# Performance work log

Measured on AMD Instinct MI355X. Metric: run time of the kernel, lower is better.

Reference implementation:

```python
import jax, jax.numpy as jnp
import numpy as np

B, H, W, C = 2, 192, 192, 192
WS, SHIFT, NH = 16, 8, 6


def _window_partition(x, ws):
    b, h, w, c = x.shape
    x = x.reshape(b, h // ws, ws, w // ws, ws, c)
    return x.transpose(0, 1, 3, 2, 4, 5).reshape(-1, ws, ws, c)


def _window_reverse(win, ws, h, w):
    b = win.shape[0] // ((h // ws) * (w // ws))
    x = win.reshape(b, h // ws, w // ws, ws, ws, -1)
    return x.transpose(0, 1, 3, 2, 4, 5).reshape(b, h, w, -1)


def _relative_position_index(ws):
    coords = np.stack(np.meshgrid(np.arange(ws), np.arange(ws), indexing="ij"))
    cf = coords.reshape(2, -1)
    rel = (cf[:, :, None] - cf[:, None, :]).transpose(1, 2, 0).astype(np.int64)
    rel[..., 0] += ws - 1
    rel[..., 1] += ws - 1
    rel[..., 0] *= 2 * ws - 1
    return rel.sum(-1)  # (ws*ws, ws*ws) in [0, (2ws-1)^2)


def _shift_attn_mask(h, w, ws, shift):
    img = np.zeros((1, h, w, 1), np.float32)
    cnt = 0
    for hs in (slice(0, -ws), slice(-ws, -shift), slice(-shift, None)):
        for wsl in (slice(0, -ws), slice(-ws, -shift), slice(-shift, None)):
            img[:, hs, wsl, :] = cnt
            cnt += 1
    mw = np.asarray(_window_partition(jnp.asarray(img), ws)).reshape(-1, ws * ws)
    diff = mw[:, None, :] - mw[:, :, None]
    return jnp.asarray(np.where(diff != 0, -100.0, 0.0).astype(np.float32))


def setup_inputs():
    key = jax.random.key(0)
    ks = jax.random.split(key, 4)
    x = jax.random.normal(ks[0], (B, H, W, C), jnp.float32)
    qkv = jax.random.normal(ks[1], (B, H, W, 3 * C), jnp.float32)
    rpb_table = 0.02 * jax.random.normal(ks[2], ((2 * WS - 1) ** 2, NH), jnp.float32)
    geo_scale = jnp.full((NH,), 0.01, jnp.float32)
    geo_sigma = jnp.asarray(1.0, jnp.float32)
    proj_w = 0.02 * jax.random.normal(ks[3], (C, C), jnp.float32)
    proj_b = jnp.zeros((C,), jnp.float32)
    rpi = jnp.asarray(_relative_position_index(WS), jnp.int32)
    attn_mask = _shift_attn_mask(H, W, WS, SHIFT)
    return dict(x=x, qkv=qkv, rpb_table=rpb_table, geo_scale=geo_scale,
                geo_sigma=geo_sigma, proj_w=proj_w, proj_b=proj_b,
                rpi=rpi, attn_mask=attn_mask,
                window_size=WS, shift_size=SHIFT, num_heads=NH)


def _geo_bias(f, ws, sigma):
    # f: (nwb, ws, ws, C). L-shaped geodesic path: horizontal then vertical cumsums.
    nwb = f.shape[0]
    diff_h = jnp.sum(jnp.abs(f[:, :, 1:] - f[:, :, :-1]), -1)  # (nwb, ws, ws-1)
    ct_h = jnp.cumsum(jnp.concatenate(
        [jnp.zeros((nwb, ws, 1), f.dtype), 1.0 + sigma * diff_h], -1), -1)
    diff_v = jnp.sum(jnp.abs(f[:, 1:] - f[:, :-1]), -1)        # (nwb, ws-1, ws)
    ct_v = jnp.cumsum(jnp.concatenate(
        [jnp.zeros((nwb, 1, ws), f.dtype), 1.0 + sigma * diff_v], -2), -2)
    idx = jnp.arange(ws * ws)
    rows, cols = idx // ws, idx % ws
    ct_h_flat = ct_h[:, rows, cols]                    # (nwb, n)
    ct_v_flat = ct_v[:, rows, cols]
    ct_h_corner = ct_h[:, rows[:, None], cols[None, :]]  # ct_h[ri, cj] -> (nwb, n, n)
    ct_v_corner = ct_v[:, rows[:, None], cols[None, :]]
    geo_h = jnp.abs(ct_h_corner - ct_h_flat[:, :, None])
    geo_v = jnp.abs(ct_v_flat[:, None, :] - ct_v_corner)
    return geo_h + geo_v                               # (nwb, n, n)


def _forward(x, qkv, rpb_table, geo_scale, geo_sigma, proj_w, proj_b,
             rpi, attn_mask, ws, shift, nh):
    b, h, w, c = x.shape
    n = ws * ws
    hd = c // nh
    sx = jnp.roll(x, (-shift, -shift), (1, 2))
    sqkv = jnp.roll(qkv, (-shift, -shift), (1, 2))
    f_win = _window_partition(sx, ws)                           # (nwb, ws, ws, c)
    geo = _geo_bias(f_win, ws, jnp.abs(geo_sigma))              # (nwb, n, n)
    qkv_win = _window_partition(sqkv, ws).reshape(-1, n, 3, nh, hd)
    q = qkv_win[:, :, 0].transpose(0, 2, 1, 3)                  # (nwb, nh, n, hd)
    k = qkv_win[:, :, 1].transpose(0, 2, 1, 3)
    v = qkv_win[:, :, 2].transpose(0, 2, 1, 3)
    attn = jnp.einsum("bhqd,bhkd->bhqk", q * (hd ** -0.5), k)   # (nwb, nh, n, n)
    rpb = rpb_table[rpi.reshape(-1)].reshape(n, n, nh).transpose(2, 0, 1)
    attn = attn + rpb[None]
    attn = attn - geo[:, None] * geo_scale[None, :, None, None]
    nw = attn_mask.shape[0]
    attn = attn.reshape(b, nw, nh, n, n) + attn_mask[None, :, None]
    attn = jax.nn.softmax(attn.reshape(-1, nh, n, n), axis=-1)
    out = jnp.einsum("bhqk,bhkd->bqhd", attn, v).reshape(-1, n, c)
    out = out @ proj_w.T + proj_b                               # nn.Linear
    out = _window_reverse(out.reshape(-1, ws, ws, c), ws, h, w)
    out = jnp.roll(out, (shift, shift), (1, 2))
    return out.reshape(b, h * w, c)


def reference(x, qkv, rpb_table, geo_scale, geo_sigma, proj_w, proj_b,
              rpi, attn_mask, window_size, shift_size, num_heads):
    return _forward(x, qkv, rpb_table, geo_scale, geo_sigma, proj_w, proj_b,
                    rpi, attn_mask, window_size, shift_size, num_heads)
```

## Files before the change

kernel.cpp:

```cpp
#include <hip/hip_runtime.h>
#include <stdint.h>

#define HH 192
#define WWW 192
#define CC 192
#define WS 16
#define SHIFTS 8
#define NH 6
#define HD 32
#define NN 256
#define NWS 12
#define NWIN_B 144
#define NWIN 288
#define CTN (NWIN * NN)

typedef _Float16 half_t;
typedef half_t half2_t __attribute__((ext_vector_type(2)));
typedef half_t f16x8 __attribute__((ext_vector_type(8)));
typedef float f32x4 __attribute__((ext_vector_type(4)));

#define LOG2E 1.4426950408889634f

#if __has_builtin(__builtin_amdgcn_exp2f)
#define EXP2F(x) __builtin_amdgcn_exp2f(x)
#else
#define EXP2F(x) __expf(0.6931471805599453f * (x))
#endif

__device__ __forceinline__ float sat16(float a) {
    return fminf(fmaxf(a, -60000.f), 60000.f);
}
__device__ __forceinline__ uint32_t pack_h2(float a, float b) {
    half2_t h; h.x = (half_t)sat16(a); h.y = (half_t)sat16(b);
    return __builtin_bit_cast(uint32_t, h);
}

__device__ __forceinline__ size_t xrow(int b, int sh, int sw) {
    int oh = sh + SHIFTS; if (oh >= HH) oh -= HH;
    int ow = sw + SHIFTS; if (ow >= WWW) ow -= WWW;
    return ((size_t)((b * HH + oh) * WWW + ow)) * CC;
}
__device__ __forceinline__ size_t qkvrow(int b, int sh, int sw) {
    int oh = sh + SHIFTS; if (oh >= HH) oh -= HH;
    int ow = sw + SHIFTS; if (ow >= WWW) ow -= WWW;
    return ((size_t)((b * HH + oh) * WWW + ow)) * (3 * CC);
}
__device__ __forceinline__ int regof(int v) { return v < (HH - WS) ? 0 : (v < (HH - SHIFTS) ? 1 : 2); }

__device__ __forceinline__ float* ctptr(float* o, int q) {
    int slot = q / 96;
    int off = q - slot * 96;
    return o + (size_t)slot * CC + 96 + off;
}

__global__ __launch_bounds__(256) void kgeo(const float* __restrict__ x,
                                            const float* __restrict__ sigp,
                                            float* __restrict__ outbuf) {
    __shared__ float dh[16][16];
    __shared__ float dv[16][16];
    int win = blockIdx.x;
    int b = win / NWIN_B, wi = win % NWIN_B;
    int wr = wi / NWS, wc = wi % NWS;
    int t = threadIdx.x;
    int r = t >> 4, j = t & 15;
    int r1 = (r < 15) ? r + 1 : r;
    int j1 = (j < 15) ? j + 1 : j;

    const float4* a4 = (const float4*)(x + xrow(b, wr * WS + r,  wc * WS + j));
    const float4* b4 = (const float4*)(x + xrow(b, wr * WS + r,  wc * WS + j1));
    const float4* c4 = (const float4*)(x + xrow(b, wr * WS + r1, wc * WS + j));
    float sh_ = 0.f, sv_ = 0.f;
    #pragma unroll 4
    for (int ch = 0; ch < 48; ch++) {
        float4 fa = a4[ch], fb = b4[ch], fc = c4[ch];
        sh_ += fabsf(fb.x - fa.x) + fabsf(fb.y - fa.y) + fabsf(fb.z - fa.z) + fabsf(fb.w - fa.w);
        sv_ += fabsf(fc.x - fa.x) + fabsf(fc.y - fa.y) + fabsf(fc.z - fa.z) + fabsf(fc.w - fa.w);
    }
    dh[r][j] = (j < 15) ? sh_ : 0.f;
    dv[r][j] = (r < 15) ? sv_ : 0.f;
    __syncthreads();

    float sigma = fabsf(sigp[0]);
    if (t < 16) {
        float acc = 0.f;
        *ctptr(outbuf, win * NN + t * 16) = 0.f;
        for (int jj = 1; jj < 16; jj++) {
            acc += 1.0f + sigma * dh[t][jj - 1];
            *ctptr(outbuf, win * NN + t * 16 + jj) = acc;
        }
    } else if (t < 32) {
        int c = t - 16;
        float acc = 0.f;
        *ctptr(outbuf, CTN + win * NN + c) = 0.f;
        for (int ii = 1; ii < 16; ii++) {
            acc += 1.0f + sigma * dv[ii - 1][c];
            *ctptr(outbuf, CTN + win * NN + ii * 16 + c) = acc;
        }
    }
}

__global__ __launch_bounds__(512, 4) void kattn(const float* __restrict__ qkv,
                                                const float* __restrict__ rpb_table,
                                                const float* __restrict__ geo_scale,
                                                float* __restrict__ outbuf) {
    __shared__ __align__(16) uint32_t Klds[256 * 20];
    __shared__ __align__(16) uint32_t Vt[32 * 140];
    __shared__ __align__(16) uint32_t Pbuf[8 * 32 * 20];
    __shared__ float cth_s[NN], ctv_s[NN];
    __shared__ float rpb_s[961];

    int win = blockIdx.x, head = blockIdx.y;
    int b = win / NWIN_B, wi = win % NWIN_B;
    int wr = wi / NWS, wc = wi % NWS;
    int wr16 = wr * WS, wc16 = wc * WS;
    int t = threadIdx.x;
    int dl = t & 15;
    int g = (t >> 4) & 3;
    int w = t >> 6;

    for (int i = t; i < 961; i += 512) rpb_s[i] = rpb_table[i * NH + head] * LOG2E;

    if (t < 256) {
        int r = t >> 4, c = t & 15;
        const float4* k4 = (const float4*)(qkv + qkvrow(b, wr16 + r, wc16 + c) + CC + head * HD);
        uint32_t kp[16];
        #pragma unroll
        for (int c4 = 0; c4 < 8; c4++) {
            float4 u = k4[c4];
            kp[c4 * 2 + 0] = pack_h2(u.x, u.y);
            kp[c4 * 2 + 1] = pack_h2(u.z, u.w);
        }
        uint4* dst = (uint4*)((char*)Klds + t * 80);
        #pragma unroll
        for (int i = 0; i < 4; i++)
            dst[i] = make_uint4(kp[i * 4 + 0], kp[i * 4 + 1], kp[i * 4 + 2], kp[i * 4 + 3]);
    } else if (t < 384) {
        int tv = t - 256;
        int p0 = 2 * tv, p1 = 2 * tv + 1;
        const float4* v0 = (const float4*)(qkv + qkvrow(b, wr16 + (p0 >> 4), wc16 + (p0 & 15)) + 2 * CC + head * HD);
        const float4* v1 = (const float4*)(qkv + qkvrow(b, wr16 + (p1 >> 4), wc16 + (p1 & 15)) + 2 * CC + head * HD);
        #pragma unroll
        for (int c4 = 0; c4 < 8; c4++) {
            float4 a = v0[c4], bu = v1[c4];
            Vt[(c4 * 4 + 0) * 140 + tv] = pack_h2(a.x, bu.x);
            Vt[(c4 * 4 + 1) * 140 + tv] = pack_h2(a.y, bu.y);
            Vt[(c4 * 4 + 2) * 140 + tv] = pack_h2(a.z, bu.z);
            Vt[(c4 * 4 + 3) * 140 + tv] = pack_h2(a.w, bu.w);
        }
    } else {
        int tc = t - 384;
        cth_s[tc]       = *ctptr(outbuf, win * NN + tc);
        cth_s[tc + 128] = *ctptr(outbuf, win * NN + tc + 128);
        ctv_s[tc]       = *ctptr(outbuf, CTN + win * NN + tc);
        ctv_s[tc + 128] = *ctptr(outbuf, CTN + win * NN + tc + 128);
    }
    f16x8 qf[2];
    #pragma unroll
    for (int qt = 0; qt < 2; qt++) {
        const float* qp = qkv + qkvrow(b, wr16 + 2 * w + qt, wc16 + dl) + head * HD + g * 8;
        float4 u0 = ((const float4*)qp)[0];
        float4 u1 = ((const float4*)qp)[1];
        f16x8 q8;
        q8[0] = (half_t)sat16(u0.x); q8[1] = (half_t)sat16(u0.y);
        q8[2] = (half_t)sat16(u0.z); q8[3] = (half_t)sat16(u0.w);
        q8[4] = (half_t)sat16(u1.x); q8[5] = (half_t)sat16(u1.y);
        q8[6] = (half_t)sat16(u1.z); q8[7] = (half_t)sat16(u1.w);
        qf[qt] = q8;
    }
    __syncthreads();

    float gscale2 = geo_scale[head] * LOG2E;
    float cvq[2], gh[8];
    int regq[8];
    #pragma unroll
    for (int qt = 0; qt < 2; qt++) {
        int rq = 2 * w + qt;
        float chq = cth_s[rq * 16 + dl];
        cvq[qt] = ctv_s[rq * 16 + dl];
        int regr = 3 * regof(wr16 + rq);
        #pragma unroll
        for (int r = 0; r < 4; r++) {
            int cq = g * 4 + r;
            gh[qt * 4 + r] = -gscale2 * fabsf(chq - cth_s[rq * 16 + cq]);
            regq[qt * 4 + r] = regr + regof(wc16 + cq);
        }
    }
    int regk_c = regof(wc16 + dl);
    const float scale2 = 0.17677669529663687f * LOG2E;

    f32x4 o[2][2];
    #pragma unroll
    for (int qt = 0; qt < 2; qt++) { o[qt][0] = (f32x4){0.f,0.f,0.f,0.f}; o[qt][1] = (f32x4){0.f,0.f,0.f,0.f}; }
    float l8[8];
    #pragma unroll
    for (int i = 0; i < 8; i++) l8[i] = 0.f;

    char* PB = (char*)Pbuf + w * 2560;
    const char* KB = (const char*)Klds;
    const char* VB = (const char*)Vt;
    const f32x4 zf = {0.f, 0.f, 0.f, 0.f};

    #pragma unroll 2
    for (int kvb = 0; kvb < 8; kvb++) {
        int kv0 = kvb * 32;
        f16x8 bk0 = *(const f16x8*)(KB + (size_t)(kv0 + dl) * 80 + g * 16);
        f16x8 bk1 = *(const f16x8*)(KB + (size_t)(kv0 + 16 + dl) * 80 + g * 16);

        f32x4 s[2][2];
        #pragma unroll
        for (int qt = 0; qt < 2; qt++) {
            s[qt][0] = __builtin_amdgcn_mfma_f32_16x16x32_f16(qf[qt], bk0, zf, 0, 0, 0);
            s[qt][1] = __builtin_amdgcn_mfma_f32_16x16x32_f16(qf[qt], bk1, zf, 0, 0, 0);
        }

        float vka = ctv_s[kv0 + dl];
        float vkb = ctv_s[kv0 + 16 + dl];
        #pragma unroll
        for (int kt = 0; kt < 2; kt++) {
            int rk = kvb * 2 + kt;
            int regk = 3 * regof(wr16 + rk) + regk_c;
            float vkk = kt ? vkb : vka;
            int kb31 = rk * 31 + dl;
            #pragma unroll
            for (int qt = 0; qt < 2; qt++) {
                float gq = -gscale2 * fabsf(vkk - cvq[qt]);
                int idxb = (2 * w + qt) * 31 + g * 4 + 480 - kb31;
                #pragma unroll
                for (int r = 0; r < 4; r++) {
                    float bias = rpb_s[idxb + r] + gh[qt * 4 + r] + gq
                               + ((regk == regq[qt * 4 + r]) ? 0.f : -100.f * LOG2E);
                    float tt = fmaf(s[qt][kt][r], scale2, bias);
                    tt = fminf(fmaxf(tt, -1000.f), 15.f);
                    float p = EXP2F(tt);
                    l8[qt * 4 + r] += p;
                    *(half_t*)(PB + (qt * 16 + g * 4 + r) * 80 + (kt * 16 + dl) * 2) = (half_t)p;
                }
            }
        }

        f16x8 bv0 = *(const f16x8*)(VB + (size_t)dl * 560 + kv0 * 2 + g * 16);
        f16x8 bv1 = *(const f16x8*)(VB + (size_t)(16 + dl) * 560 + kv0 * 2 + g * 16);
        #pragma unroll
        for (int qt = 0; qt < 2; qt++) {
            f16x8 ap = *(const f16x8*)(PB + (qt * 16 + dl) * 80 + g * 16);
            o[qt][0] = __builtin_amdgcn_mfma_f32_16x16x32_f16(ap, bv0, o[qt][0], 0, 0, 0);
            o[qt][1] = __builtin_amdgcn_mfma_f32_16x16x32_f16(ap, bv1, o[qt][1], 0, 0, 0);
        }
    }

    float inv[8];
    #pragma unroll
    for (int i = 0; i < 8; i++) {
        float li = l8[i];
        li += __shfl_xor(li, 1);
        li += __shfl_xor(li, 2);
        li += __shfl_xor(li, 4);
        li += __shfl_xor(li, 8);
        inv[i] = 1.0f / li;
    }

    #pragma unroll
    for (int qt = 0; qt < 2; qt++)
        #pragma unroll
        for (int dt = 0; dt < 2; dt++)
            #pragma unroll
            for (int r = 0; r < 4; r++) {
                float val = o[qt][dt][r] * inv[qt * 4 + r];
                *(half_t*)(PB + (qt * 16 + g * 4 + r) * 80 + (dt * 16 + dl) * 2) = (half_t)sat16(val);
            }

    int lane = t & 63;
    int lp = lane >> 1, half = lane & 1;
    int tok = 32 * w + lp;
    int rr = tok >> 4, pc = tok & 15;
    int oh = wr16 + rr + SHIFTS; if (oh >= HH) oh -= HH;
    int ow = wc16 + pc + SHIFTS; if (ow >= WWW) ow -= WWW;
    size_t R = (size_t)b * (HH * WWW) + (size_t)oh * WWW + ow;
    uint4* o4p = (uint4*)outbuf;
    const uint4* src = (const uint4*)(PB + lp * 80 + half * 32);
    size_t base4 = R * 48 + head * 4 + half * 2;
    o4p[base4 + 0] = src[0];
    o4p[base4 + 1] = src[1];
}

__global__ __launch_bounds__(512, 4) void kproj(float* __restrict__ data,
                                                const float* __restrict__ proj_w,
                                                const float* __restrict__ proj_b) {
    __shared__ __align__(16) uint32_t Wh[192 * 100];
    int t = threadIdx.x;
    size_t R0 = (size_t)blockIdx.x * 128;

    const float4* pw4 = (const float4*)proj_w;
    for (int q = t; q < 9216; q += 512) {
        int j = q / 48, c4 = q - j * 48;
        float4 u = pw4[q];
        *(uint2*)&Wh[j * 100 + c4 * 2] = make_uint2(pack_h2(u.x, u.y), pack_h2(u.z, u.w));
    }
    __syncthreads();

    int dl = t & 15, g = (t >> 4) & 3, w = t >> 6;
    const char* WB = (const char*)Wh;
    const char* AB = (const char*)data;

    f32x4 acc[12];
    #pragma unroll
    for (int i = 0; i < 12; i++) acc[i] = (f32x4){0.f, 0.f, 0.f, 0.f};

    size_t arow = (size_t)(R0 + w * 16 + dl) * 768;
    #pragma unroll
    for (int ch = 0; ch < 6; ch++) {
        f16x8 af = *(const f16x8*)(AB + arow + ch * 64 + g * 16);
        #pragma unroll
        for (int jt = 0; jt < 12; jt++) {
            f16x8 bf = *(const f16x8*)(WB + (size_t)(jt * 16 + dl) * 400 + ch * 64 + g * 16);
            acc[jt] = __builtin_amdgcn_mfma_f32_16x16x32_f16(af, bf, acc[jt], 0, 0, 0);
        }
    }

    float bvv[12];
    #pragma unroll
    for (int jt = 0; jt < 12; jt++) bvv[jt] = proj_b[jt * 16 + dl];
    size_t orow = (size_t)(R0 + w * 16 + g * 4) * 192;
    #pragma unroll
    for (int jt = 0; jt < 12; jt++)
        #pragma unroll
        for (int r = 0; r < 4; r++)
            data[orow + (size_t)r * 192 + jt * 16 + dl] = acc[jt][r] + bvv[jt];
}

extern "C" void kernel_launch(void* const* d_in, const int* in_sizes, int n_in,
                              void* d_out, int out_size, void* d_ws, size_t ws_size,
                              hipStream_t stream) {
    const float *x = nullptr, *qkv = nullptr, *rpb = nullptr, *gsc = nullptr,
                *pw = nullptr, *pb = nullptr, *sig = nullptr;
    for (int i = 0; i < n_in; i++) {
        switch (in_sizes[i]) {
            case 14155776: x   = (const float*)d_in[i]; break;
            case 42467328: qkv = (const float*)d_in[i]; break;
            case 5766:     rpb = (const float*)d_in[i]; break;
            case 6:        gsc = (const float*)d_in[i]; break;
            case 36864:    pw  = (const float*)d_in[i]; break;
            case 192:      pb  = (const float*)d_in[i]; break;
            default: break;
        }
    }
    if (n_in > 4 && in_sizes[4] == 1) sig = (const float*)d_in[4];
    else for (int i = 0; i < n_in; i++) if (in_sizes[i] == 1) { sig = (const float*)d_in[i]; break; }
    if (!x)   x   = (const float*)d_in[0];
    if (!qkv) qkv = (const float*)d_in[1];
    if (!rpb) rpb = (const float*)d_in[2];
    if (!gsc) gsc = (const float*)d_in[3];
    if (!sig) sig = (const float*)d_in[4];
    if (!pw)  pw  = (const float*)d_in[5];
    if (!pb)  pb  = (const float*)d_in[6];

    float* out = (float*)d_out;

    kgeo<<<dim3(NWIN), dim3(256), 0, stream>>>(x, sig, out);
    kattn<<<dim3(NWIN, NH), dim3(512), 0, stream>>>(qkv, rpb, gsc, out);
    kproj<<<dim3((NWIN * NN) / 128), dim3(512), 0, stream>>>(out, pw, pb);
}
```

Baseline: 405.6 us.

## Compute transposed S=K·Q^T and feed P to PV MFMA via shuffles instead of LDS

```diff
diff --git a/kernel.cpp b/kernel.cpp
--- a/kernel.cpp
+++ b/kernel.cpp
@@ -18,6 +18,7 @@
 typedef half_t half2_t __attribute__((ext_vector_type(2)));
 typedef half_t f16x8 __attribute__((ext_vector_type(8)));
 typedef float f32x4 __attribute__((ext_vector_type(4)));
+typedef uint32_t u32x4 __attribute__((ext_vector_type(4)));
 
 #define LOG2E 1.4426950408889634f
 
@@ -32,6 +33,10 @@
 }
 __device__ __forceinline__ uint32_t pack_h2(float a, float b) {
     half2_t h; h.x = (half_t)sat16(a); h.y = (half_t)sat16(b);
+    return __builtin_bit_cast(uint32_t, h);
+}
+__device__ __forceinline__ uint32_t pack_p(float a, float b) {
+    half2_t h; h.x = (half_t)a; h.y = (half_t)b;
     return __builtin_bit_cast(uint32_t, h);
 }
 
@@ -99,14 +104,14 @@
     }
 }
 
-__global__ __launch_bounds__(512, 4) void kattn(const float* __restrict__ qkv,
+__global__ __launch_bounds__(512, 6) void kattn(const float* __restrict__ qkv,
                                                 const float* __restrict__ rpb_table,
                                                 const float* __restrict__ geo_scale,
                                                 float* __restrict__ outbuf) {
     __shared__ __align__(16) uint32_t Klds[256 * 20];
     __shared__ __align__(16) uint32_t Vt[32 * 140];
-    __shared__ __align__(16) uint32_t Pbuf[8 * 32 * 20];
-    __shared__ float cth_s[NN], ctv_s[NN];
+    __shared__ __align__(16) float cth_s[NN];
+    __shared__ __align__(16) float ctv_s[NN];
     __shared__ float rpb_s[961];
 
     int win = blockIdx.x, head = blockIdx.y;
@@ -116,6 +121,7 @@
     int t = threadIdx.x;
     int dl = t & 15;
     int g = (t >> 4) & 3;
+    int g4 = g * 4;
     int w = t >> 6;
 
     for (int i = t; i < 961; i += 512) rpb_s[i] = rpb_table[i * NH + head] * LOG2E;
@@ -170,103 +176,119 @@
     __syncthreads();
 
     float gscale2 = geo_scale[head] * LOG2E;
-    float cvq[2], gh[8];
-    int regq[8];
+    float ghs[2][4];
+    f32x4 Dv[2];
+    int regq[2], qb0[2];
     #pragma unroll
     for (int qt = 0; qt < 2; qt++) {
         int rq = 2 * w + qt;
         float chq = cth_s[rq * 16 + dl];
-        cvq[qt] = ctv_s[rq * 16 + dl];
-        int regr = 3 * regof(wr16 + rq);
-        #pragma unroll
-        for (int r = 0; r < 4; r++) {
-            int cq = g * 4 + r;
-            gh[qt * 4 + r] = -gscale2 * fabsf(chq - cth_s[rq * 16 + cq]);
-            regq[qt * 4 + r] = regr + regof(wc16 + cq);
-        }
-    }
-    int regk_c = regof(wc16 + dl);
+        f32x4 Bv = *(const f32x4*)&cth_s[rq * 16 + g4];
+        Dv[qt] = *(const f32x4*)&ctv_s[rq * 16 + g4];
+        #pragma unroll
+        for (int r = 0; r < 4; r++) ghs[qt][r] = -gscale2 * fabsf(Bv[r] - chq);
+        regq[qt] = 3 * regof(wr16 + rq) + regof(wc16 + dl);
+        qb0[qt] = rq * 31 + dl + 480 - g4;
+    }
+    int regkc[4];
+    #pragma unroll
+    for (int r = 0; r < 4; r++) regkc[r] = regof(wc16 + g4 + r);
     const float scale2 = 0.17677669529663687f * LOG2E;
 
     f32x4 o[2][2];
     #pragma unroll
     for (int qt = 0; qt < 2; qt++) { o[qt][0] = (f32x4){0.f,0.f,0.f,0.f}; o[qt][1] = (f32x4){0.f,0.f,0.f,0.f}; }
-    float l8[8];
-    #pragma unroll
-    for (int i = 0; i < 8; i++) l8[i] = 0.f;
-
-    char* PB = (char*)Pbuf + w * 2560;
+    float lq[2] = {0.f, 0.f};
+
     const char* KB = (const char*)Klds;
     const char* VB = (const char*)Vt;
     const f32x4 zf = {0.f, 0.f, 0.f, 0.f};
+    int srcA = ((g & 1) << 5) + dl;
+    int srcB = srcA + 16;
+    bool hi = (g >= 2);
 
     #pragma unroll 2
     for (int kvb = 0; kvb < 8; kvb++) {
         int kv0 = kvb * 32;
-        f16x8 bk0 = *(const f16x8*)(KB + (size_t)(kv0 + dl) * 80 + g * 16);
-        f16x8 bk1 = *(const f16x8*)(KB + (size_t)(kv0 + 16 + dl) * 80 + g * 16);
+        f16x8 ak0 = *(const f16x8*)(KB + (size_t)(kv0 + dl) * 80 + g * 16);
+        f16x8 ak1 = *(const f16x8*)(KB + (size_t)(kv0 + 16 + dl) * 80 + g * 16);
 
         f32x4 s[2][2];
         #pragma unroll
         for (int qt = 0; qt < 2; qt++) {
-            s[qt][0] = __builtin_amdgcn_mfma_f32_16x16x32_f16(qf[qt], bk0, zf, 0, 0, 0);
-            s[qt][1] = __builtin_amdgcn_mfma_f32_16x16x32_f16(qf[qt], bk1, zf, 0, 0, 0);
-        }
-
-        float vka = ctv_s[kv0 + dl];
-        float vkb = ctv_s[kv0 + 16 + dl];
-        #pragma unroll
-        for (int kt = 0; kt < 2; kt++) {
-            int rk = kvb * 2 + kt;
-            int regk = 3 * regof(wr16 + rk) + regk_c;
-            float vkk = kt ? vkb : vka;
-            int kb31 = rk * 31 + dl;
+            s[qt][0] = __builtin_amdgcn_mfma_f32_16x16x32_f16(ak0, qf[qt], zf, 0, 0, 0);
+            s[qt][1] = __builtin_amdgcn_mfma_f32_16x16x32_f16(ak1, qf[qt], zf, 0, 0, 0);
+        }
+
+        f32x4 cv0 = *(const f32x4*)&ctv_s[kv0 + g4];
+        f32x4 cv1 = *(const f32x4*)&ctv_s[kv0 + 16 + g4];
+        int rowreg0 = 3 * regof(wr16 + kvb * 2);
+        int rowreg1 = 3 * regof(wr16 + kvb * 2 + 1);
+
+        uint32_t pkk[2][2][2];
+        #pragma unroll
+        for (int qt = 0; qt < 2; qt++) {
             #pragma unroll
-            for (int qt = 0; qt < 2; qt++) {
-                float gq = -gscale2 * fabsf(vkk - cvq[qt]);
-                int idxb = (2 * w + qt) * 31 + g * 4 + 480 - kb31;
+            for (int kt = 0; kt < 2; kt++) {
+                int rowreg = kt ? rowreg1 : rowreg0;
+                int idxk = qb0[qt] - (kvb * 2 + kt) * 31;
+                float pr[4];
                 #pragma unroll
                 for (int r = 0; r < 4; r++) {
-                    float bias = rpb_s[idxb + r] + gh[qt * 4 + r] + gq
-                               + ((regk == regq[qt * 4 + r]) ? 0.f : -100.f * LOG2E);
-                    float tt = fmaf(s[qt][kt][r], scale2, bias);
+                    float C = kt ? cv1[r] : cv0[r];
+                    float geoV = fabsf(C - Dv[qt][r]);
+                    float bias = rpb_s[idxk - r] + ghs[qt][r]
+                               + ((rowreg + regkc[r] == regq[qt]) ? 0.f : -100.f * LOG2E);
+                    float tt = fmaf(s[qt][kt][r], scale2, fmaf(-gscale2, geoV, bias));
                     tt = fminf(fmaxf(tt, -1000.f), 15.f);
                     float p = EXP2F(tt);
-                    l8[qt * 4 + r] += p;
-                    *(half_t*)(PB + (qt * 16 + g * 4 + r) * 80 + (kt * 16 + dl) * 2) = (half_t)p;
+                    lq[qt] += p;
+                    pr[r] = p;
                 }
+                pkk[qt][kt][0] = pack_p(pr[0], pr[1]);
+                pkk[qt][kt][1] = pack_p(pr[2], pr[3]);
             }
         }
 
         f16x8 bv0 = *(const f16x8*)(VB + (size_t)dl * 560 + kv0 * 2 + g * 16);
         f16x8 bv1 = *(const f16x8*)(VB + (size_t)(16 + dl) * 560 + kv0 * 2 + g * 16);
+
         #pragma unroll
         for (int qt = 0; qt < 2; qt++) {
-            f16x8 ap = *(const f16x8*)(PB + (qt * 16 + dl) * 80 + g * 16);
+            uint32_t a00 = __shfl((int)pkk[qt][0][0], srcA), a01 = __shfl((int)pkk[qt][0][1], srcA);
+            uint32_t a10 = __shfl((int)pkk[qt][0][0], srcB), a11 = __shfl((int)pkk[qt][0][1], srcB);
+            uint32_t b00 = __shfl((int)pkk[qt][1][0], srcA), b01 = __shfl((int)pkk[qt][1][1], srcA);
+            uint32_t b10 = __shfl((int)pkk[qt][1][0], srcB), b11 = __shfl((int)pkk[qt][1][1], srcB);
+            u32x4 uu;
+            uu.x = hi ? b00 : a00; uu.y = hi ? b01 : a01;
+            uu.z = hi ? b10 : a10; uu.w = hi ? b11 : a11;
+            f16x8 ap = __builtin_bit_cast(f16x8, uu);
             o[qt][0] = __builtin_amdgcn_mfma_f32_16x16x32_f16(ap, bv0, o[qt][0], 0, 0, 0);
             o[qt][1] = __builtin_amdgcn_mfma_f32_16x16x32_f16(ap, bv1, o[qt][1], 0, 0, 0);
         }
     }
 
-    float inv[8];
-    #pragma unroll
-    for (int i = 0; i < 8; i++) {
-        float li = l8[i];
-        li += __shfl_xor(li, 1);
-        li += __shfl_xor(li, 2);
-        li += __shfl_xor(li, 4);
-        li += __shfl_xor(li, 8);
-        inv[i] = 1.0f / li;
-    }
-
+    float invr[2][4];
+    #pragma unroll
+    for (int qt = 0; qt < 2; qt++) {
+        float li = lq[qt];
+        li += __shfl_xor(li, 16);
+        li += __shfl_xor(li, 32);
+        float iv = 1.0f / li;
+        #pragma unroll
+        for (int r = 0; r < 4; r++) invr[qt][r] = __shfl(iv, g4 + r);
+    }
+
+    __syncthreads();
+    char* OB = (char*)Klds + w * 2560;
     #pragma unroll
     for (int qt = 0; qt < 2; qt++)
         #pragma unroll
         for (int dt = 0; dt < 2; dt++)
             #pragma unroll
             for (int r = 0; r < 4; r++) {
-                float val = o[qt][dt][r] * inv[qt * 4 + r];
-                *(half_t*)(PB + (qt * 16 + g * 4 + r) * 80 + (dt * 16 + dl) * 2) = (half_t)sat16(val);
+                float val = o[qt][dt][r] * invr[qt][r];
+                *(half_t*)(OB + (qt * 16 + g4 + r) * 80 + (dt * 16 + dl) * 2) = (half_t)sat16(val);
             }
 
     int lane = t & 63;
@@ -277,7 +299,7 @@
     int ow = wc16 + pc + SHIFTS; if (ow >= WWW) ow -= WWW;
     size_t R = (size_t)b * (HH * WWW) + (size_t)oh * WWW + ow;
     uint4* o4p = (uint4*)outbuf;
-    const uint4* src = (const uint4*)(PB + lp * 80 + half * 32);
+    const uint4* src = (const uint4*)(OB + lp * 80 + half * 32);
     size_t base4 = R * 48 + head * 4 + half * 2;
     o4p[base4 + 0] = src[0];
     o4p[base4 + 1] = src[1];
```

After: 580.4 us. +43.1%, slower.
